# Kernel optimization log

Hardware: AMD Instinct MI355X
Metric: run time of the kernel (lower is better)

Reference implementation:

```python
import jax, jax.numpy as jnp
import numpy as np
from jax import lax

C_LIGHT = 3e8
SPATIAL, CROP = 64, 128
BIN_LEN, WALL, SAMP_COEFF, CYCLES = 0.01, 2.0, 2.0, 5
B, D = 2, 1


def _waveconvparam(bin_resolution, virtual_wavelength, cycles):
    samples = int(round(cycles * virtual_wavelength / (C_LIGHT * bin_resolution)))
    num_cycles = samples * (C_LIGHT * bin_resolution) / virtual_wavelength
    sigma = 0.3
    g = np.arange(samples, dtype=np.float64)
    env = np.exp(-(((g - samples / 2.0) / (samples / 2.0)) ** 2) / (2 * sigma ** 2))
    cos_k = np.cos(2 * np.pi * num_cycles * g / samples) * env
    sin_k = np.sin(2 * np.pi * num_cycles * g / samples) * env
    return cos_k, sin_k


def _define_psf(N, M, slope):
    # LCT psf: locus of min |(4 slope)^2 (x^2+y^2) - z|, normalized and circularly shifted
    x = np.arange(2 * N, dtype=np.float64) / (2 * N - 1) * 2 - 1
    z = np.arange(2 * M, dtype=np.float64) / (2 * M - 1) * 2
    gy, gx, gz = np.meshgrid(x, x, z)  # (2N,2N,2M)
    blur = np.abs((4 * slope) ** 2 * (gx ** 2 + gy ** 2) - gz)
    d = (np.abs(blur - blur.min(axis=2, keepdims=True)) < 1e-8).astype(np.float64)
    e = d / np.sqrt(d.sum())
    f = np.roll(np.roll(e, N, axis=0), N, axis=1)
    return np.transpose(f, (2, 0, 1))  # (2M,2N,2N)


def _resampling_operator(M):
    row = M * M
    x = np.arange(1, row + 1, dtype=np.float64)
    mtx = np.zeros((row, M), dtype=np.float64)
    mtx[np.arange(row), np.ceil(np.sqrt(x)).astype(np.int64) - 1] = 1.0
    mtx = mtx / np.sqrt(x)[:, None]
    mtxi = mtx.T.copy()
    for _ in range(int(np.log2(M))):
        mtx = 0.5 * (mtx[0::2] + mtx[1::2])
        mtxi = 0.5 * (mtxi[:, 0::2] + mtxi[:, 1::2])
    return mtx.astype(np.float32), mtxi.astype(np.float32)


def setup_inputs() -> dict:
    key = jax.random.key(0)
    kf, kw, kb = jax.random.split(key, 3)
    bin_res = BIN_LEN / C_LIGHT
    trange = CROP * C_LIGHT * bin_res
    slope = (WALL / 2.0) / trange
    vlam = SAMP_COEFF * 2.0 * (WALL / (SPATIAL - 1))
    cos_k, sin_k = _waveconvparam(bin_res, vlam, CYCLES)
    wave = np.stack([cos_k, sin_k], 0)[:, ::-1][:, None, :].astype(np.float32)  # (2,1,k)
    psf = _define_psf(SPATIAL, CROP, slope)
    invpsf = np.conj(np.fft.fftn(psf))
    mtx, mtxi = _resampling_operator(CROP)
    return {
        "feature": jax.random.normal(kf, (B, D, CROP, SPATIAL, SPATIAL), jnp.float32),
        "conv_w": jax.random.normal(kw, ()) * 0.1 + 1.0,
        "conv_b": jax.random.normal(kb, ()) * 0.1,
        "wave": jnp.asarray(wave),
        "invpsf_real": jnp.asarray(np.real(invpsf).astype(np.float32))[None],
        "invpsf_imag": jnp.asarray(np.imag(invpsf).astype(np.float32))[None],
        "mtx": jnp.asarray(mtx),
        "mtxi": jnp.asarray(mtxi),
    }


def _attention(k1, k2, w, b):
    # SE-style cross attention; Conv3d(1,1,1) on unbatched (C=1,T,H,W) is w*x+b
    T = k2.shape[1]
    pe = jnp.sin(jnp.arange(T, dtype=k2.dtype))  # PE3D with 1 channel -> sin along T
    k2p = k2 + pe[None, :, None, None]
    scal = jnp.mean(w * k1 + b)  # conv + adaptive_avg_pool3d(1), channel dim = 1
    q = (w * k2p + b).reshape(1, 1, -1)
    attn = jax.nn.sigmoid(jax.nn.softmax(scal * q, axis=2)).reshape(k2p.shape)
    return attn * k2p


def _fre_atten2(kernel, w, b):
    _, T, H, W = kernel.shape
    ct, ch, cw = T // 2, H // 2, W // 2
    st, sh, sw = (T - ct) // 2, (H - ch) // 2, (W - cw) // 2
    sl = (slice(None), slice(ct - st, ct + st), slice(ch - sh, ch + sh), slice(cw - sw, cw + sw))
    high = kernel[sl]
    low = jnp.roll(kernel, (ct, ch, cw), axis=(1, 2, 3))[sl]
    l2l = _attention(low, low, w, b)
    l2h = _attention(l2l, high, w, b)
    temp = kernel.at[sl].set(l2h)
    temp = jnp.roll(temp, (ct, ch, cw), axis=(1, 2, 3)).at[sl].set(l2l)
    return jnp.roll(temp, (ct, ch, cw), axis=(1, 2, 3))


def _forward(feature, conv_w, conv_b, wave, invpsf_real, invpsf_imag, mtx, mtxi):
    b, d, T, H, W = feature.shape
    BD = b * d
    k = wave.shape[2]
    # virtual wave conv along time: (BDHW,1,T) x (2,1,k)
    data = feature.reshape(BD, T, H, W).transpose(0, 2, 3, 1).reshape(-1, 1, T)
    conv = lax.conv_general_dilated(data, wave, (1,), [(k // 2, k // 2)],
                                    dimension_numbers=("NCH", "OIH", "NCH"))
    if k % 2 == 0:
        conv = conv[:, :, 1:]
    data2 = conv.reshape(BD, H, W, 2, T).transpose(3, 0, 4, 1, 2).reshape(2 * BD, T, H, W)
    # temporal resampling then zero-pad to 2T,2H,2W
    tmp = jnp.einsum("tm,bmx->btx", mtx, data2.reshape(2 * BD, T, H * W)).reshape(2 * BD, T, H, W)
    datapad = jnp.zeros((2 * BD, 2 * T, 2 * H, 2 * W), feature.dtype).at[:, :T, :H, :W].set(tmp)
    datafre = jnp.fft.fftn(datapad)  # torch.fft.fftn transforms ALL dims incl. batch
    w1 = _fre_atten2(invpsf_real, conv_w, conv_b)
    w2 = _fre_atten2(invpsf_imag, conv_w, conv_b)
    re_real = datafre.real * w1 - datafre.imag * w2
    re_imag = datafre.real * w2 + datafre.imag * w1
    re = jnp.fft.ifftn(lax.complex(re_real, re_imag))
    vol = re[:, :T, :H, :W]
    cr, ci = vol[:BD].real, vol[:BD].imag
    sr, si = vol[BD:].real, vol[BD:].imag
    sum_real = cr ** 2 - ci ** 2 + sr ** 2 - si ** 2
    sum_imag = 2 * cr * ci + 2 * sr * si
    mag = jax.nn.relu((jnp.sqrt(sum_real ** 2 + sum_imag ** 2) + sum_real) * 0.5)
    sq = jnp.sqrt(mag)
    out = jnp.einsum("tm,bmx->btx", mtxi, sq.reshape(BD, T, H * W))
    return out.reshape(b, d, T, H, W)


def reference(feature, conv_w, conv_b, wave, invpsf_real, invpsf_imag, mtx, mtxi):
    return _forward(feature, conv_w, conv_b, wave, invpsf_real, invpsf_imag, mtx, mtxi)
```

## Files before the change

kernel.cpp:

```cpp
#include <hip/hip_runtime.h>

#define BLKE 524288
#define VOLE 4194304
#define TCROP 2097152
#define PI2 6.283185307179586476925286766559

__device__ __forceinline__ float2 cmulf(float2 a, float2 b){
  return make_float2(a.x*b.x - a.y*b.y, a.x*b.y + a.y*b.x);
}
__device__ __forceinline__ float waveSum(float v){
  #pragma unroll
  for (int o=32;o;o>>=1) v += __shfl_xor(v,o);
  return v;
}
__device__ __forceinline__ float waveMaxf(float v){
  #pragma unroll
  for (int o=32;o;o>>=1) v = fmaxf(v,__shfl_xor(v,o));
  return v;
}
__device__ __forceinline__ float waveMinf(float v){
  #pragma unroll
  for (int o=32;o;o>>=1) v = fminf(v,__shfl_xor(v,o));
  return v;
}

__device__ __forceinline__ void bcastReduce5(const float* __restrict__ pA, int kap,
    float& sum, float& mnl, float& mxl, float& mnh, float& mxh, float* sm ){
  int tid = threadIdx.x;
  const float* q = pA + kap*1280 + tid*5;
  float s = q[0], a = q[1], b = q[2], c = q[3], d = q[4];
  s = waveSum(s); a = waveMinf(a); b = waveMaxf(b); c = waveMinf(c); d = waveMaxf(d);
  if ((tid&63)==0){ int w = tid>>6; sm[w]=s; sm[4+w]=a; sm[8+w]=b; sm[12+w]=c; sm[16+w]=d; }
  __syncthreads();
  sum = sm[0]+sm[1]+sm[2]+sm[3];
  mnl = fminf(fminf(sm[4],sm[5]),fminf(sm[6],sm[7]));
  mxl = fmaxf(fmaxf(sm[8],sm[9]),fmaxf(sm[10],sm[11]));
  mnh = fminf(fminf(sm[12],sm[13]),fminf(sm[14],sm[15]));
  mxh = fmaxf(fmaxf(sm[16],sm[17]),fmaxf(sm[18],sm[19]));
}

__device__ __forceinline__ float bcastSum256(const float* __restrict__ p, float* sm ){
  int tid = threadIdx.x;
  float s = waveSum(p[tid]);
  if ((tid&63)==0) sm[tid>>6] = s;
  __syncthreads();
  return sm[0]+sm[1]+sm[2]+sm[3];
}

__global__ void __launch_bounds__(256) kD1(const float* __restrict__ mtx,
                                           const float* __restrict__ wave,
                                           float* __restrict__ M,
                                           const float* __restrict__ Kr,
                                           const float* __restrict__ Ki,
                                           float* __restrict__ Lw, float* __restrict__ Hw,
                                           float* __restrict__ pA,
                                           float2* __restrict__ twF,
                                           float2* __restrict__ twD,
                                           float2* __restrict__ twI){
  __shared__ float spe[128];
  __shared__ float sm[20];
  int bid = blockIdx.x;
  int tid = threadIdx.x;
  if (bid < 512){
    int kap = bid >> 8, bx = bid & 255;
    const float* K = kap ? Ki : Kr;
    if (tid < 128) spe[tid] = sinf((float)tid);
    __syncthreads();
    float sum=0.f, mnl=3.4e38f, mxl=-3.4e38f, mnh=3.4e38f, mxh=-3.4e38f;
    int base = bx*256 + tid;
    #pragma unroll
    for (int it = 0; it < 8; it++){
      int e = base + it*65536;
      int tau = e >> 12, rem = e & 4095, eta = rem >> 6, om = rem & 63;
      float pe = spe[tau];
      float lo = K[(size_t)((tau+192)&255)*16384 + ((eta+96)&127)*128 + ((om+96)&127)];
      float hi = K[(size_t)(tau+64)*16384 + (eta+32)*128 + (om+32)];
      sum += lo;
      float lp = lo+pe, hp = hi+pe;
      Lw[kap*BLKE + e] = lp;
      Hw[kap*BLKE + e] = hp;
      mnl=fminf(mnl,lp); mxl=fmaxf(mxl,lp);
      mnh=fminf(mnh,hp); mxh=fmaxf(mxh,hp);
    }
    sum = waveSum(sum); mnl=waveMinf(mnl); mxl=waveMaxf(mxl); mnh=waveMinf(mnh); mxh=waveMaxf(mxh);
    if ((tid&63)==0){ int w=tid>>6; sm[w]=sum; sm[4+w]=mnl; sm[8+w]=mxl; sm[12+w]=mnh; sm[16+w]=mxh; }
    __syncthreads();
    if (tid==0){
      float* o = pA + kap*1280 + bx*5;
      o[0] = sm[0]+sm[1]+sm[2]+sm[3];
      o[1] = fminf(fminf(sm[4],sm[5]),fminf(sm[6],sm[7]));
      o[2] = fmaxf(fmaxf(sm[8],sm[9]),fmaxf(sm[10],sm[11]));
      o[3] = fminf(fminf(sm[12],sm[13]),fminf(sm[14],sm[15]));
      o[4] = fmaxf(fmaxf(sm[16],sm[17]),fmaxf(sm[18],sm[19]));
    }
  } else if (bid < 640){
    int idx = (bid-512)*256 + tid;
    int o = idx >> 14, r = idx & 16383;
    int t = r >> 7, s = r & 127;
    float acc = 0.f;
    int mlo = s-31; if (mlo < 0) mlo = 0;
    int mhi = s+31; if (mhi > 127) mhi = 127;
    for (int m = mlo; m <= mhi; m++) acc += mtx[t*128+m]*wave[o*63 + (s-m+31)];
    M[idx] = acc;
  } else {
    if (tid < 256){
      double ang = -PI2 * (double)tid / 256.0;
      twF[tid] = make_float2((float)cos(ang), (float)sin(ang));
    }
    if (tid < 64){
      double a2 = -PI2 * (double)tid / 128.0;
      twD[tid] = make_float2((float)cos(a2), (float)sin(a2));
      double a3 =  PI2 * (double)tid / 128.0;
      twI[tid] = make_float2((float)cos(a3), (float)sin(a3));
    }
  }
}

__global__ void __launch_bounds__(256) kD2(const float* __restrict__ feat,
                                           const float* __restrict__ M,
                                           float* __restrict__ tmp,
                                           const float* __restrict__ pA,
                                           const float* __restrict__ Lw,
                                           float* __restrict__ pB,
                                           const float* cw, const float* cb){
  __shared__ __align__(16) char smem[16640];
  __shared__ float sm[20], smo[4];
  int bid = blockIdx.x;
  int tid = threadIdx.x;
  if (bid < 512){
    int kap = bid >> 8, bx = bid & 255;
    float sum,mnl,mxl,mnh,mxh;
    bcastReduce5(pA,kap,sum,mnl,mxl,mnh,mxh,sm);
    float w = cw[0], b = cb[0];
    float s1 = w*(sum*(1.0f/BLKE)) + b;
    float a1 = s1*w, c1 = s1*b;
    float mx = (a1>=0.f) ? a1*mxl+c1 : a1*mnl+c1;
    float acc = 0.f;
    int base = kap*BLKE + bx*256 + tid;
    #pragma unroll
    for (int it = 0; it < 8; it++){
      float lp = Lw[base + it*65536];
      acc += expf(a1*lp + c1 - mx);
    }
    acc = waveSum(acc);
    if ((tid&63)==0) smo[tid>>6] = acc;
    __syncthreads();
    if (tid==0) pB[kap*256 + bx] = smo[0]+smo[1]+smo[2]+smo[3];
  } else {
    int e = bid - 512;
    int b = e >> 8, tt = (e >> 6) & 3, xt = e & 63;
    float (*LF)[64] = (float(*)[64])smem;
    float (*LM)[32][33] = (float(*)[32][33])(smem + 8192);
    int xx = tid & 63, tq = tid >> 6;
    float acc0[8] = {}, acc1[8] = {};
    const float* fb = feat + (size_t)b*BLKE;
    for (int sb = 0; sb < 4; sb++){
      #pragma unroll
      for (int j = 0; j < 8; j++){
        int idx = tid + j*256; int s = idx >> 6, x = idx & 63;
        LF[s][x] = fb[(size_t)(sb*32+s)*4096 + xt*64 + x];
      }
      #pragma unroll
      for (int j = 0; j < 8; j++){
        int idx = tid + j*256; int o = idx >> 10, r = idx & 1023;
        int trow = r >> 5, s = r & 31;
        LM[o][trow][s] = M[o*16384 + (tt*32+trow)*128 + sb*32+s];
      }
      __syncthreads();
      for (int s = 0; s < 32; s++){
        float f = LF[s][xx];
        #pragma unroll
        for (int i = 0; i < 8; i++){
          acc0[i] += LM[0][tq*8+i][s]*f;
          acc1[i] += LM[1][tq*8+i][s]*f;
        }
      }
      __syncthreads();
    }
    #pragma unroll
    for (int i = 0; i < 8; i++){
      int t = tt*32 + tq*8 + i;
      tmp[(size_t)(0*2+b)*BLKE + (size_t)t*4096 + xt*64+xx] = acc0[i];
      tmp[(size_t)(1*2+b)*BLKE + (size_t)t*4096 + xt*64+xx] = acc1[i];
    }
  }
}

__global__ void __launch_bounds__(256) kD3(const float* __restrict__ tmp,
                                           float2* __restrict__ Z2,
                                           const float* __restrict__ pA,
                                           const float* __restrict__ pB,
                                           const float* __restrict__ Lw,
                                           float* __restrict__ pC,
                                           const float* cw, const float* cb,
                                           const float2* __restrict__ twg){
  __shared__ __align__(16) char smem[8832];
  __shared__ float sm[20], smB[4], smo[4];
  int bid = blockIdx.x;
  int tid = threadIdx.x;
  if (bid < 512){
    int kap = bid >> 8, bx = bid & 255;
    float sum,mnl,mxl,mnh,mxh;
    bcastReduce5(pA,kap,sum,mnl,mxl,mnh,mxh,sm);
    float d1 = bcastSum256(pB + kap*256, smB);
    float w = cw[0], b = cb[0];
    float s1 = w*(sum*(1.0f/BLKE)) + b;
    float a1 = s1*w, c1 = s1*b;
    float mx = (a1>=0.f) ? a1*mxl+c1 : a1*mnl+c1;
    float invd = 1.0f/d1;
    float acc = 0.f;
    int base = kap*BLKE + bx*256 + tid;
    #pragma unroll
    for (int it = 0; it < 8; it++){
      float lp = Lw[base + it*65536];
      float p = expf(a1*lp + c1 - mx)*invd;
      acc += lp/(1.f + expf(-p));
    }
    acc = waveSum(acc);
    if ((tid&63)==0) smo[tid>>6] = acc;
    __syncthreads();
    if (tid==0) pC[kap*256 + bx] = smo[0]+smo[1]+smo[2]+smo[3];
  } else {
    int e = bid - 512;
    int b = e >> 11, bx = e & 2047;
    float2 (*bA)[130] = (float2(*)[130])smem;
    float2 (*bB)[130] = (float2(*)[130])(smem + 4160);
    float2* tw = (float2*)(smem + 8320);
    if (tid < 64) tw[tid] = twg[tid];
    int l = tid >> 6, lane = tid & 63;
    int line = bx*4 + l;
    int t = line >> 6, h = line & 63;
    const float* pc = tmp + (size_t)b*BLKE + (size_t)t*4096 + h*64;
    const float* ps = tmp + (size_t)(2+b)*BLKE + (size_t)t*4096 + h*64;
    bA[l][lane] = make_float2(pc[lane], ps[lane]);
    bA[l][lane+64] = make_float2(0.f, 0.f);
    __syncthreads();
    float2 (*src)[130] = bA, (*dst)[130] = bB;
    int m = 1;
    #pragma unroll
    for (int st = 0; st < 7; st++){
      int i = lane;
      int jm = i & ~(m-1);
      float2 a = src[l][i], b2 = src[l][i+64];
      float2 s = make_float2(a.x+b2.x, a.y+b2.y);
      float2 d = make_float2(a.x-b2.x, a.y-b2.y);
      dst[l][i+jm]   = s;
      dst[l][i+jm+m] = cmulf(d, tw[jm]);
      __syncthreads();
      float2 (*tp)[130] = src; src = dst; dst = tp;
      m <<= 1;
    }
    float2* outp = Z2 + (size_t)b*TCROP + (size_t)t*16384 + (size_t)h*128;
    outp[lane]    = src[l][lane];
    outp[lane+64] = src[l][lane+64];
  }
}

__global__ void __launch_bounds__(256) kD4(float2* __restrict__ Z2,
                                           const float* __restrict__ pA,
                                           const float* __restrict__ pC,
                                           const float* __restrict__ Hw,
                                           float* __restrict__ pD,
                                           const float* cw, const float* cb,
                                           const float2* __restrict__ twg){
  __shared__ __align__(16) char smem[33792];
  __shared__ float sm[20], smC[4], smo[4];
  int bid = blockIdx.x;
  int tid = threadIdx.x;
  if (bid < 512){
    int kap = bid >> 8, bx = bid & 255;
    float sum,mnl,mxl,mnh,mxh;
    bcastReduce5(pA,kap,sum,mnl,mxl,mnh,mxh,sm);
    float sl2 = bcastSum256(pC + kap*256, smC);
    float w = cw[0], b = cb[0];
    float s2 = w*(sl2*(1.0f/BLKE)) + b;
    float a2 = s2*w, c2 = s2*b;
    float mx = (a2>=0.f) ? a2*mxh+c2 : a2*mnh+c2;
    float acc = 0.f;
    int base = kap*BLKE + bx*256 + tid;
    #pragma unroll
    for (int it = 0; it < 8; it++){
      float hp = Hw[base + it*65536];
      acc += expf(a2*hp + c2 - mx);
    }
    acc = waveSum(acc);
    if ((tid&63)==0) smo[tid>>6] = acc;
    __syncthreads();
    if (tid==0) pD[kap*256 + bx] = smo[0]+smo[1]+smo[2]+smo[3];
  } else {
    int e = bid - 512;
    int b = e >> 10, bx = e & 1023;
    float2 (*bA)[130] = (float2(*)[130])smem;
    float2 (*bB)[130] = (float2(*)[130])(smem + 16640);
    float2* tw = (float2*)(smem + 33280);
    if (tid < 64) tw[tid] = twg[tid];
    float2* Z = Z2 + (size_t)b*TCROP;
    int t = bx >> 3; int w0 = (bx & 7) << 4;
    size_t base = (size_t)t*16384 + w0;
    #pragma unroll
    for (int q = 0; q < 4; q++){
      int idx = q*256 + tid; int wl = idx & 15, hh = idx >> 4;
      bA[wl][hh] = Z[base + (size_t)hh*128 + wl];
      bA[wl][hh+64] = make_float2(0.f, 0.f);
    }
    __syncthreads();
    float2 (*src)[130] = bA, (*dst)[130] = bB;
    int m = 1;
    #pragma unroll
    for (int st = 0; st < 7; st++){
      #pragma unroll
      for (int q = 0; q < 4; q++){
        int g = q*256 + tid; int li = g >> 6; int i = g & 63;
        int jm = i & ~(m-1);
        float2 a = src[li][i], b2 = src[li][i+64];
        float2 s = make_float2(a.x+b2.x, a.y+b2.y);
        float2 d = make_float2(a.x-b2.x, a.y-b2.y);
        dst[li][i+jm]   = s;
        dst[li][i+jm+m] = cmulf(d, tw[jm]);
      }
      __syncthreads();
      float2 (*tp)[130] = src; src = dst; dst = tp;
      m <<= 1;
    }
    #pragma unroll
    for (int q = 0; q < 8; q++){
      int idx = q*256 + tid; int wl = idx & 15, hh = idx >> 4;
      Z[base + (size_t)hh*128 + wl] = src[wl][hh];
    }
  }
}

__device__ __forceinline__ float attnv(float v, float a, float c, float mx, float invd){
  float p = expf(a*v + c - mx)*invd;
  return v / (1.f + expf(-p));
}
__device__ __forceinline__ float2 wcAt(int t, int h, int w,
                                       const float* __restrict__ Kr, const float* __restrict__ Ki,
                                       const float* spe, const float* P){
  size_t off = (size_t)t*16384 + (size_t)h*128 + w;
  float kr = Kr[off], ki = Ki[off];
  bool center = (t>=64 && t<192) && (h>=32 && h<96) && (w>=32 && w<96);
  int tc = (t+64)&255, hc = (h+32)&127, wc = (w+32)&127;
  bool corner = (tc<128) && (hc<64) && (wc<64);
  bool act = center || corner;
  float pe = spe[(center ? (t-64) : tc) & 127];
  float A0 = center?P[4]:P[0],   C0 = center?P[5]:P[1];
  float M0 = center?P[6]:P[2],   I0 = center?P[7]:P[3];
  float A1 = center?P[12]:P[8],  C1 = center?P[13]:P[9];
  float M1 = center?P[14]:P[10], I1 = center?P[15]:P[11];
  float ox = attnv(kr+pe, A0, C0, M0, I0);
  float oy = attnv(ki+pe, A1, C1, M1, I1);
  return make_float2(act?ox:kr, act?oy:ki);
}

__global__ void __launch_bounds__(256) kP(const float* __restrict__ pA,
                                          const float* __restrict__ pB,
                                          const float* __restrict__ pC,
                                          const float* __restrict__ pD,
                                          const float* cw, const float* cb,
                                          float* __restrict__ Pg){
  __shared__ float sm[20], smB[4], smC[4], smD[4];
  int tid = threadIdx.x;
  for (int kap = 0; kap < 2; kap++){
    if (kap) __syncthreads();
    float sum,mnl,mxl,mnh,mxh;
    bcastReduce5(pA,kap,sum,mnl,mxl,mnh,mxh,sm);
    float d1  = bcastSum256(pB + kap*256, smB);
    float sl2 = bcastSum256(pC + kap*256, smC);
    float d2  = bcastSum256(pD + kap*256, smD);
    if (tid==0){
      float w = cw[0], b = cb[0];
      float s1 = w*(sum*(1.0f/BLKE)) + b;
      float a1 = s1*w, c1 = s1*b;
      float mx1 = (a1>=0.f) ? a1*mxl+c1 : a1*mnl+c1;
      float s2 = w*(sl2*(1.0f/BLKE)) + b;
      float a2 = s2*w, c2 = s2*b;
      float mx2 = (a2>=0.f) ? a2*mxh+c2 : a2*mnh+c2;
      float* Q = Pg + kap*8;
      Q[0]=a1; Q[1]=c1; Q[2]=mx1; Q[3]=1.0f/d1;
      Q[4]=a2; Q[5]=c2; Q[6]=mx2; Q[7]=1.0f/d2;
    }
  }
}

__global__ void __launch_bounds__(256) kWc(const float* __restrict__ Kr,
                                           const float* __restrict__ Ki,
                                           const float* __restrict__ Pg,
                                           float2* __restrict__ Wc){
  __shared__ float spe[128];
  __shared__ float P[16];
  int tid = threadIdx.x;
  if (tid < 128) spe[tid] = sinf((float)tid);
  else if (tid < 144) P[tid-128] = Pg[tid-128];
  __syncthreads();
  #pragma unroll
  for (int q = 0; q < 4; q++){
    int idx = blockIdx.x*1024 + q*256 + tid;
    int t = idx >> 14, r = idx & 16383, h = r >> 7, w = r & 127;
    Wc[idx] = wcAt(t, h, w, Kr, Ki, spe, P);
  }
}

__global__ void __launch_bounds__(512) kTfused(const float2* __restrict__ Z2,
                                               float2* __restrict__ U2,
                                               float2* __restrict__ V2,
                                               const float2* __restrict__ Wc,
                                               const float2* __restrict__ twg){
  __shared__ float2 buf[16][259];
  __shared__ float2 tw[256];
  int tid = threadIdx.x;
  if (tid < 256) tw[tid] = twg[tid];
  int b = blockIdx.y;
  int bid = blockIdx.x;
  int h = bid >> 3, w0 = (bid & 7) << 4;
  int wl = tid & 15, pq = tid >> 4;
  const float2* Z = Z2 + (size_t)b*TCROP;
  size_t gbase = (size_t)h*128 + w0 + wl;
  #pragma unroll
  for (int q = 0; q < 4; q++){
    int p = q*32 + pq;
    buf[wl][p] = Z[(size_t)p*16384 + gbase];
    buf[wl][p+128] = make_float2(0.f, 0.f);
  }
  __syncthreads();
  #pragma unroll
  for (int st = 0; st < 4; st++){
    const int Q = 64 >> (2*st);
    const int f = 1 << (2*st);
    #pragma unroll
    for (int it = 0; it < 2; it++){
      int u = pq + 32*it;
      int j = u & (Q-1);
      int seg = u >> (6 - 2*st);
      int base = (seg << (8 - 2*st)) + j;
      float2 a0 = buf[wl][base];
      float2 a1 = buf[wl][base+Q];
      float2 a2 = buf[wl][base+2*Q];
      float2 a3 = buf[wl][base+3*Q];
      float2 t0 = make_float2(a0.x+a2.x, a0.y+a2.y);
      float2 t1 = make_float2(a0.x-a2.x, a0.y-a2.y);
      float2 t2 = make_float2(a1.x+a3.x, a1.y+a3.y);
      float2 t3 = make_float2(a1.x-a3.x, a1.y-a3.y);
      float2 z0 = make_float2(t0.x+t2.x, t0.y+t2.y);
      float2 z2 = make_float2(t0.x-t2.x, t0.y-t2.y);
      float2 z1 = make_float2(t1.x+t3.y, t1.y-t3.x);
      float2 z3 = make_float2(t1.x-t3.y, t1.y+t3.x);
      buf[wl][base]     = z0;
      buf[wl][base+Q]   = cmulf(z1, tw[f*j]);
      buf[wl][base+2*Q] = cmulf(z2, tw[2*f*j]);
      buf[wl][base+3*Q] = cmulf(z3, tw[3*f*j]);
    }
    __syncthreads();
  }
  float2 rg[8];
  #pragma unroll
  for (int q = 0; q < 8; q++) rg[q] = buf[wl][q*32 + pq];
  #pragma unroll
  for (int q = 0; q < 8; q++){
    int p = q*32 + pq;
    int kt = ((p&3)<<6) | (((p>>2)&3)<<4) | (((p>>4)&3)<<2) | ((p>>6)&3);
    float2 wc = Wc[(size_t)kt*16384 + (size_t)h*128 + w0 + wl];
    buf[wl][p] = cmulf(rg[q], wc);
  }
  __syncthreads();
  #pragma unroll
  for (int st = 0; st < 4; st++){
    const int Q = 1 << (2*st);
    const int f = 64 >> (2*st);
    #pragma unroll
    for (int it = 0; it < 2; it++){
      int u = pq + 32*it;
      int j = u & (Q-1);
      int seg = u >> (2*st);
      int base = (seg << (2*st + 2)) + j;
      float2 w1 = tw[f*j], w2 = tw[2*f*j], w3 = tw[3*f*j];
      float2 a0 = buf[wl][base];
      float2 r1 = buf[wl][base+Q];
      float2 r2 = buf[wl][base+2*Q];
      float2 r3 = buf[wl][base+3*Q];
      float2 b1 = make_float2(r1.x*w1.x + r1.y*w1.y, r1.y*w1.x - r1.x*w1.y);
      float2 b2 = make_float2(r2.x*w2.x + r2.y*w2.y, r2.y*w2.x - r2.x*w2.y);
      float2 b3 = make_float2(r3.x*w3.x + r3.y*w3.y, r3.y*w3.x - r3.x*w3.y);
      float2 t0 = make_float2(a0.x+b2.x, a0.y+b2.y);
      float2 t1 = make_float2(a0.x-b2.x, a0.y-b2.y);
      float2 t2 = make_float2(b1.x+b3.x, b1.y+b3.y);
      float2 t3 = make_float2(b1.x-b3.x, b1.y-b3.y);
      buf[wl][base]     = make_float2(t0.x+t2.x, t0.y+t2.y);
      buf[wl][base+Q]   = make_float2(t1.x-t3.y, t1.y+t3.x);
      buf[wl][base+2*Q] = make_float2(t0.x-t2.x, t0.y-t2.y);
      buf[wl][base+3*Q] = make_float2(t1.x+t3.y, t1.y-t3.x);
    }
    __syncthreads();
  }
  float2* Uo = U2 + (size_t)b*TCROP;
  #pragma unroll
  for (int q = 0; q < 4; q++){
    int p = q*32 + pq;
    Uo[(size_t)p*16384 + gbase] = buf[wl][p];
  }
  #pragma unroll
  for (int q = 0; q < 8; q++){
    int p = q*32 + pq;
    int kt = ((p&3)<<6) | (((p>>2)&3)<<4) | (((p>>4)&3)<<2) | ((p>>6)&3);
    int tm = (256-kt)&255, hm = (128-h)&127, wm = (128-(w0+wl))&127;
    float2 wc = Wc[(size_t)tm*16384 + (size_t)hm*128 + wm];
    wc.y = -wc.y;
    buf[wl][p] = cmulf(rg[q], wc);
  }
  __syncthreads();
  #pragma unroll
  for (int st = 0; st < 4; st++){
    const int Q = 1 << (2*st);
    const int f = 64 >> (2*st);
    #pragma unroll
    for (int it = 0; it < 2; it++){
      int u = pq + 32*it;
      int j = u & (Q-1);
      int seg = u >> (2*st);
      int base = (seg << (2*st + 2)) + j;
      float2 w1 = tw[f*j], w2 = tw[2*f*j], w3 = tw[3*f*j];
      float2 a0 = buf[wl][base];
      float2 r1 = buf[wl][base+Q];
      float2 r2 = buf[wl][base+2*Q];
      float2 r3 = buf[wl][base+3*Q];
      float2 b1 = make_float2(r1.x*w1.x + r1.y*w1.y, r1.y*w1.x - r1.x*w1.y);
      float2 b2 = make_float2(r2.x*w2.x + r2.y*w2.y, r2.y*w2.x - r2.x*w2.y);
      float2 b3 = make_float2(r3.x*w3.x + r3.y*w3.y, r3.y*w3.x - r3.x*w3.y);
      float2 t0 = make_float2(a0.x+b2.x, a0.y+b2.y);
      float2 t1 = make_float2(a0.x-b2.x, a0.y-b2.y);
      float2 t2 = make_float2(b1.x+b3.x, b1.y+b3.y);
      float2 t3 = make_float2(b1.x-b3.x, b1.y-b3.y);
      buf[wl][base]     = make_float2(t0.x+t2.x, t0.y+t2.y);
      buf[wl][base+Q]   = make_float2(t1.x-t3.y, t1.y+t3.x);
      buf[wl][base+2*Q] = make_float2(t0.x-t2.x, t0.y-t2.y);
      buf[wl][base+3*Q] = make_float2(t1.x+t3.y, t1.y-t3.x);
    }
    __syncthreads();
  }
  float2* Vo = V2 + (size_t)b*TCROP;
  #pragma unroll
  for (int q = 0; q < 4; q++){
    int p = q*32 + pq;
    Vo[(size_t)p*16384 + gbase] = buf[wl][p];
  }
}

__global__ void __launch_bounds__(512,8) kHi(float2* __restrict__ U2, float2* __restrict__ V2,
                                             const float2* __restrict__ twg){
  __shared__ float2 bA[16][130], bB[16][130], tw[64];
  int tid = threadIdx.x;
  if (tid < 64) tw[tid] = twg[tid];
  float2* Z = (blockIdx.z ? V2 : U2) + (size_t)blockIdx.y*TCROP;
  int bid = blockIdx.x;
  int t = bid >> 3; int w0 = (bid & 7) << 4;
  size_t base = (size_t)t*16384 + w0;
  #pragma unroll
  for (int q = 0; q < 4; q++){
    int idx = q*512 + tid; int wl = idx & 15, hh = idx >> 4;
    bA[wl][hh] = Z[base + (size_t)hh*128 + wl];
  }
  __syncthreads();
  float2 (*src)[130] = bA, (*dst)[130] = bB;
  int m = 1;
  #pragma unroll
  for (int st = 0; st < 7; st++){
    #pragma unroll
    for (int q = 0; q < 2; q++){
      int g = q*512 + tid; int li = g >> 6; int i = g & 63;
      int jm = i & ~(m-1);
      float2 a = src[li][i], b2 = src[li][i+64];
      float2 s = make_float2(a.x+b2.x, a.y+b2.y);
      float2 d = make_float2(a.x-b2.x, a.y-b2.y);
      dst[li][i+jm]   = s;
      dst[li][i+jm+m] = cmulf(d, tw[jm]);
    }
    __syncthreads();
    float2 (*tp)[130] = src; src = dst; dst = tp;
    m <<= 1;
  }
  #pragma unroll
  for (int q = 0; q < 2; q++){
    int idx = q*512 + tid; int wl = idx & 15, hh = idx >> 4;
    Z[base + (size_t)hh*128 + wl] = src[wl][hh];
  }
}

__global__ void __launch_bounds__(256) kI3C(const float2* __restrict__ U2,
                                            const float2* __restrict__ V2,
                                            float* __restrict__ sq,
                                            const float2* __restrict__ twg){
  __shared__ float2 bA[4][130], bB[4][130], tw[64];
  int tid = threadIdx.x;
  if (tid < 64) tw[tid] = twg[tid];
  int b = blockIdx.y;
  int l = tid >> 6, lane = tid & 63;
  int line = blockIdx.x*4 + l;
  int t = line >> 6, h = line & 63;
  size_t off = (size_t)b*TCROP + (size_t)t*16384 + (size_t)h*128;
  bA[l][lane]    = U2[off + lane];
  bA[l][lane+64] = U2[off + lane + 64];
  __syncthreads();
  float2 (*src)[130] = bA, (*dst)[130] = bB;
  int m = 1;
  #pragma unroll
  for (int st = 0; st < 7; st++){
    int i = lane;
    int jm = i & ~(m-1);
    float2 a = src[l][i], b2 = src[l][i+64];
    float2 s = make_float2(a.x+b2.x, a.y+b2.y);
    float2 d = make_float2(a.x-b2.x, a.y-b2.y);
    dst[l][i+jm]   = s;
    dst[l][i+jm+m] = cmulf(d, tw[jm]);
    __syncthreads();
    float2 (*tp)[130] = src; src = dst; dst = tp;
    m <<= 1;
  }
  float2 y = src[l][lane];
  dst[l][lane]    = V2[off + lane];
  dst[l][lane+64] = V2[off + lane + 64];
  __syncthreads();
  src = dst; dst = (src == bA) ? bB : bA;
  m = 1;
  #pragma unroll
  for (int st = 0; st < 7; st++){
    int i = lane;
    int jm = i & ~(m-1);
    float2 a = src[l][i], b2 = src[l][i+64];
    float2 s = make_float2(a.x+b2.x, a.y+b2.y);
    float2 d = make_float2(a.x-b2.x, a.y-b2.y);
    dst[l][i+jm]   = s;
    dst[l][i+jm+m] = cmulf(d, tw[jm]);
    __syncthreads();
    float2 (*tp)[130] = src; src = dst; dst = tp;
    m <<= 1;
  }
  float2 v = src[l][lane];
  const float sc = 1.0f/(float)VOLE;
  const float sc2 = sc*sc;
  float2 s = cmulf(y, make_float2(v.x, -v.y));
  s.x *= sc2; s.y *= sc2;
  float mag = 0.5f*(sqrtf(s.x*s.x + s.y*s.y) + s.x);
  mag = fmaxf(mag, 0.f);
  sq[(size_t)b*BLKE + (size_t)t*4096 + h*64 + lane] = sqrtf(mag);
}

__global__ void __launch_bounds__(256) kOut(const float* __restrict__ sq,
                                            const float* __restrict__ mtxi,
                                            float* __restrict__ out){
  __shared__ float LF[32][64];
  __shared__ float LM[32][33];
  int b = blockIdx.z, tt = blockIdx.y, xt = blockIdx.x;
  int tid = threadIdx.x;
  int xx = tid & 63, tq = tid >> 6;
  float acc[8] = {};
  const float* fb = sq + (size_t)b*BLKE;
  for (int sb = 0; sb < 4; sb++){
    #pragma unroll
    for (int j = 0; j < 8; j++){
      int idx = tid + j*256; int s = idx >> 6, x = idx & 63;
      LF[s][x] = fb[(size_t)(sb*32+s)*4096 + xt*64 + x];
    }
    #pragma unroll
    for (int j = 0; j < 4; j++){
      int idx = tid + j*256; int trow = idx >> 5, s = idx & 31;
      LM[trow][s] = mtxi[(tt*32+trow)*128 + sb*32+s];
    }
    __syncthreads();
    for (int s = 0; s < 32; s++){
      float f = LF[s][xx];
      #pragma unroll
      for (int i = 0; i < 8; i++) acc[i] += LM[tq*8+i][s]*f;
    }
    __syncthreads();
  }
  #pragma unroll
  for (int i = 0; i < 8; i++){
    int t = tt*32 + tq*8 + i;
    out[(size_t)b*BLKE + (size_t)t*4096 + xt*64+xx] = acc[i];
  }
}

extern "C" void kernel_launch(void* const* d_in, const int* in_sizes, int n_in,
                              void* d_out, int out_size, void* d_ws, size_t ws_size,
                              hipStream_t stream){
  const float* feature = (const float*)d_in[0];
  const float* convW   = (const float*)d_in[1];
  const float* convB   = (const float*)d_in[2];
  const float* wave    = (const float*)d_in[3];
  const float* Kr      = (const float*)d_in[4];
  const float* Ki      = (const float*)d_in[5];
  const float* mtx     = (const float*)d_in[6];
  const float* mtxi    = (const float*)d_in[7];
  float* out = (float*)d_out;
  float* ws  = (float*)d_ws;

  float*  M    = ws;
  float*  pA   = ws + 32832;
  float*  pB   = ws + 35392;
  float*  pC   = ws + 35904;
  float*  pD   = ws + 36416;
  float*  Pg   = ws + 37440;
  float2* twF  = (float2*)(ws + 40960);
  float2* twD  = (float2*)(ws + 41472);
  float2* twI  = (float2*)(ws + 41600);
  float*  tmp  = ws + 65536;
  float*  sq   = ws + 65536 + 2097152;
  float2* Z2   = (float2*)(ws + 3211264);
  float2* U2   = (float2*)(ws + 11599872);
  float2* V2   = (float2*)(ws + 19988480);
  float2* Wc   = (float2*)(ws + 28377088);
  float*  Lw   = (float*)U2;
  float*  Hw   = ((float*)U2) + 1048576;

  kD1 <<<641,  256, 0, stream>>>(mtx, wave, M, Kr, Ki, Lw, Hw, pA, twF, twD, twI);
  kD2 <<<1024, 256, 0, stream>>>(feature, M, tmp, pA, Lw, pB, convW, convB);
  kD3 <<<4608, 256, 0, stream>>>(tmp, Z2, pA, pB, Lw, pC, convW, convB, twD);
  kD4 <<<2560, 256, 0, stream>>>(Z2, pA, pC, Hw, pD, convW, convB, twD);
  kP  <<<1,    256, 0, stream>>>(pA, pB, pC, pD, convW, convB, Pg);
  kWc <<<4096, 256, 0, stream>>>(Kr, Ki, Pg, Wc);
  kTfused<<<dim3(1024,2), 512, 0, stream>>>(Z2, U2, V2, Wc, twF);
  kHi<<<dim3(1024,2,2), 512, 0, stream>>>(U2, V2, twI);
  kI3C<<<dim3(2048,2), 256, 0, stream>>>(U2, V2, sq, twI);
  kOut<<<dim3(64,4,2), 256, 0, stream>>>(sq, mtxi, out);
}
```

Before: 263.2 us.

## Fuse inverse H and W FFT passes into one per-plane shared-memory kernel

Replaces the separate H-axis inverse FFT kernel (which wrote back to global) and the W-axis FFT plus magnitude kernel with a single kernel that loads a full 128x128 complex plane into LDS, runs both axes in place, and computes the output only for the cropped 64x64 region using bit-reversed reads. This removes a full global read and write round trip of U2/V2 and one launch. The cost is a 128 KB shared-memory tile per block, which allows only one block per CU and launches just 256 blocks, so occupancy and latency hiding are much lower.

```diff
diff --git a/kernel.cpp b/kernel.cpp
--- a/kernel.cpp
+++ b/kernel.cpp
@@ -545,103 +545,91 @@
   }
 }
 
-__global__ void __launch_bounds__(512,8) kHi(float2* __restrict__ U2, float2* __restrict__ V2,
-                                             const float2* __restrict__ twg){
-  __shared__ float2 bA[16][130], bB[16][130], tw[64];
-  int tid = threadIdx.x;
-  if (tid < 64) tw[tid] = twg[tid];
-  float2* Z = (blockIdx.z ? V2 : U2) + (size_t)blockIdx.y*TCROP;
-  int bid = blockIdx.x;
-  int t = bid >> 3; int w0 = (bid & 7) << 4;
-  size_t base = (size_t)t*16384 + w0;
-  #pragma unroll
-  for (int q = 0; q < 4; q++){
-    int idx = q*512 + tid; int wl = idx & 15, hh = idx >> 4;
-    bA[wl][hh] = Z[base + (size_t)hh*128 + wl];
-  }
-  __syncthreads();
-  float2 (*src)[130] = bA, (*dst)[130] = bB;
-  int m = 1;
-  #pragma unroll
-  for (int st = 0; st < 7; st++){
-    #pragma unroll
-    for (int q = 0; q < 2; q++){
-      int g = q*512 + tid; int li = g >> 6; int i = g & 63;
-      int jm = i & ~(m-1);
-      float2 a = src[li][i], b2 = src[li][i+64];
-      float2 s = make_float2(a.x+b2.x, a.y+b2.y);
-      float2 d = make_float2(a.x-b2.x, a.y-b2.y);
-      dst[li][i+jm]   = s;
-      dst[li][i+jm+m] = cmulf(d, tw[jm]);
-    }
-    __syncthreads();
-    float2 (*tp)[130] = src; src = dst; dst = tp;
-    m <<= 1;
-  }
-  #pragma unroll
-  for (int q = 0; q < 2; q++){
-    int idx = q*512 + tid; int wl = idx & 15, hh = idx >> 4;
-    Z[base + (size_t)hh*128 + wl] = src[wl][hh];
-  }
-}
-
-__global__ void __launch_bounds__(256) kI3C(const float2* __restrict__ U2,
+__global__ void __launch_bounds__(1024) kHW(const float2* __restrict__ U2,
                                             const float2* __restrict__ V2,
                                             float* __restrict__ sq,
                                             const float2* __restrict__ twg){
-  __shared__ float2 bA[4][130], bB[4][130], tw[64];
+  __shared__ float2 plane[16384];
+  __shared__ float2 tw[64];
   int tid = threadIdx.x;
   if (tid < 64) tw[tid] = twg[tid];
-  int b = blockIdx.y;
-  int l = tid >> 6, lane = tid & 63;
-  int line = blockIdx.x*4 + l;
-  int t = line >> 6, h = line & 63;
-  size_t off = (size_t)b*TCROP + (size_t)t*16384 + (size_t)h*128;
-  bA[l][lane]    = U2[off + lane];
-  bA[l][lane+64] = U2[off + lane + 64];
-  __syncthreads();
-  float2 (*src)[130] = bA, (*dst)[130] = bB;
-  int m = 1;
-  #pragma unroll
-  for (int st = 0; st < 7; st++){
-    int i = lane;
-    int jm = i & ~(m-1);
-    float2 a = src[l][i], b2 = src[l][i+64];
-    float2 s = make_float2(a.x+b2.x, a.y+b2.y);
-    float2 d = make_float2(a.x-b2.x, a.y-b2.y);
-    dst[l][i+jm]   = s;
-    dst[l][i+jm+m] = cmulf(d, tw[jm]);
-    __syncthreads();
-    float2 (*tp)[130] = src; src = dst; dst = tp;
-    m <<= 1;
-  }
-  float2 y = src[l][lane];
-  dst[l][lane]    = V2[off + lane];
-  dst[l][lane+64] = V2[off + lane + 64];
-  __syncthreads();
-  src = dst; dst = (src == bA) ? bB : bA;
-  m = 1;
-  #pragma unroll
-  for (int st = 0; st < 7; st++){
-    int i = lane;
-    int jm = i & ~(m-1);
-    float2 a = src[l][i], b2 = src[l][i+64];
-    float2 s = make_float2(a.x+b2.x, a.y+b2.y);
-    float2 d = make_float2(a.x-b2.x, a.y-b2.y);
-    dst[l][i+jm]   = s;
-    dst[l][i+jm+m] = cmulf(d, tw[jm]);
-    __syncthreads();
-    float2 (*tp)[130] = src; src = dst; dst = tp;
-    m <<= 1;
-  }
-  float2 v = src[l][lane];
-  const float sc = 1.0f/(float)VOLE;
-  const float sc2 = sc*sc;
-  float2 s = cmulf(y, make_float2(v.x, -v.y));
-  s.x *= sc2; s.y *= sc2;
-  float mag = 0.5f*(sqrtf(s.x*s.x + s.y*s.y) + s.x);
-  mag = fmaxf(mag, 0.f);
-  sq[(size_t)b*BLKE + (size_t)t*4096 + h*64 + lane] = sqrtf(mag);
+  int t = blockIdx.x, b = blockIdx.y;
+  size_t off = (size_t)b*TCROP + (size_t)t*16384;
+  float2 yr[4];
+  #pragma unroll
+  for (int uv = 0; uv < 2; uv++){
+    const float2* src = (uv ? V2 : U2) + off;
+    #pragma unroll
+    for (int it = 0; it < 16; it++){
+      int idx = it*1024 + tid;
+      plane[idx] = src[idx];
+    }
+    __syncthreads();
+    float4* P4 = (float4*)plane;
+    #pragma unroll
+    for (int s = 6; s >= 0; s--){
+      int m = 1 << s, sh = 6 - s;
+      #pragma unroll
+      for (int it = 0; it < 4; it++){
+        int task = it*1024 + tid;
+        int w2 = task & 63, pr = task >> 6;
+        int j = pr & (m-1);
+        int pos = ((pr & ~(m-1)) << 1) | j;
+        float4 a  = P4[pos*64 + w2];
+        float4 bq = P4[(pos+m)*64 + w2];
+        float2 twv = tw[j << sh];
+        float4 sv;
+        sv.x = a.x+bq.x; sv.y = a.y+bq.y; sv.z = a.z+bq.z; sv.w = a.w+bq.w;
+        float dx = a.x-bq.x, dy = a.y-bq.y, dz = a.z-bq.z, dw = a.w-bq.w;
+        float4 dv;
+        dv.x = dx*twv.x - dy*twv.y; dv.y = dx*twv.y + dy*twv.x;
+        dv.z = dz*twv.x - dw*twv.y; dv.w = dz*twv.y + dw*twv.x;
+        P4[pos*64 + w2]     = sv;
+        P4[(pos+m)*64 + w2] = dv;
+      }
+      __syncthreads();
+    }
+    #pragma unroll
+    for (int s = 6; s >= 0; s--){
+      int m = 1 << s, sh = 6 - s;
+      #pragma unroll
+      for (int it = 0; it < 4; it++){
+        int task = it*1024 + tid;
+        int pr = task & 63;
+        int hr = (task >> 6) << 1;
+        int j = pr & (m-1);
+        int pos = ((pr & ~(m-1)) << 1) | j;
+        float2 a  = plane[hr*128 + pos];
+        float2 bq = plane[hr*128 + pos + m];
+        float2 twv = tw[j << sh];
+        float2 d = make_float2(a.x-bq.x, a.y-bq.y);
+        plane[hr*128 + pos]     = make_float2(a.x+bq.x, a.y+bq.y);
+        plane[hr*128 + pos + m] = cmulf(d, twv);
+      }
+      __syncthreads();
+    }
+    #pragma unroll
+    for (int it = 0; it < 4; it++){
+      int oidx = it*1024 + tid;
+      int h = oidx >> 6, w = oidx & 63;
+      int hr = (int)(__brev((unsigned)h) >> 25);
+      int wr = (int)(__brev((unsigned)w) >> 25);
+      float2 v = plane[hr*128 + wr];
+      if (uv == 0){
+        yr[it] = v;
+      } else {
+        float2 y = yr[it];
+        const float sc = 1.0f/(float)VOLE;
+        const float sc2 = sc*sc;
+        float2 sv = cmulf(y, make_float2(v.x, -v.y));
+        sv.x *= sc2; sv.y *= sc2;
+        float mag = 0.5f*(sqrtf(sv.x*sv.x + sv.y*sv.y) + sv.x);
+        mag = fmaxf(mag, 0.f);
+        sq[(size_t)b*BLKE + (size_t)t*4096 + oidx] = sqrtf(mag);
+      }
+    }
+    if (uv == 0) __syncthreads();
+  }
 }
 
 __global__ void __launch_bounds__(256) kOut(const float* __restrict__ sq,
@@ -719,7 +707,6 @@
   kP  <<<1,    256, 0, stream>>>(pA, pB, pC, pD, convW, convB, Pg);
   kWc <<<4096, 256, 0, stream>>>(Kr, Ki, Pg, Wc);
   kTfused<<<dim3(1024,2), 512, 0, stream>>>(Z2, U2, V2, Wc, twF);
-  kHi<<<dim3(1024,2,2), 512, 0, stream>>>(U2, V2, twI);
-  kI3C<<<dim3(2048,2), 256, 0, stream>>>(U2, V2, sq, twI);
+  kHW<<<dim3(128,2), 1024, 0, stream>>>(U2, V2, sq, twI);
   kOut<<<dim3(64,4,2), 256, 0, stream>>>(sq, mtxi, out);
 }
```

New measurement: 268.0 us. No clear change (+1.8%).
